# Optimization experiments

Hardware: AMD Instinct MI355X
Metric: run time of the kernel (lower is better)

Reference implementation:

```python
import jax, jax.numpy as jnp
import numpy as np
import math

N = 131072   # number of points
C = 32       # embed_dim
K = 19       # num_class
ZD = 16      # z_dim
BN_EPS = 1e-4
SIG_THR = 0.8


def setup_inputs():
    key = jax.random.key(0)
    ks = jax.random.split(key, 16)
    f32 = jnp.float32
    rn = lambda k, s, sc=1.0: jax.random.normal(k, s, dtype=f32) * sc
    return {
        'feat': rn(ks[0], (N, C)),
        'scene_flow': rn(ks[1], (N, 3)),
        'coarse_pred': rn(ks[2], (N, K)),
        'z': rn(ks[3], (ZD,)),
        'select_w1': rn(ks[4], (C, C), 0.2),
        'bn_gamma': jnp.ones((C,), f32),
        'bn_beta': jnp.zeros((C,), f32),
        'bn_mean': jnp.zeros((C,), f32),
        'bn_var': jnp.ones((C,), f32),
        'select_w2': rn(ks[5], (C, 1), 0.2),
        'select_b2': jnp.zeros((1,), f32),
        'wq': rn(ks[6], (C, C), 0.2), 'bq': jnp.zeros((C,), f32),
        'wk': rn(ks[7], (C, C), 0.2), 'bk': jnp.zeros((C,), f32),
        'wv': rn(ks[8], (C, C), 0.2), 'bv': jnp.zeros((C,), f32),
        'wo': rn(ks[9], (C, C), 0.2), 'bo': jnp.zeros((C,), f32),
        'wt': rn(ks[10], (2 * C, C), 0.2), 'bt': jnp.zeros((C,), f32),
        'w_out': rn(ks[11], (C, K), 0.2), 'b_out': jnp.zeros((K,), f32),
        'w_gen': rn(ks[12], (ZD + K + 3, C), 0.2), 'b_gen': jnp.zeros((C,), f32),
    }


def _forward(feat, scene_flow, coarse_pred, z, select_w1, bn_gamma, bn_beta,
             bn_mean, bn_var, select_w2, select_b2, wq, bq, wk, bk, wv, bv,
             wo, bo, wt, bt, w_out, b_out, w_gen, b_gen):
    cp = jax.nn.softmax(coarse_pred, axis=-1)                      # (N, K)
    temp_mask = jnp.any(scene_flow != 0, axis=-1)                  # (N,)
    # select_mlp: Linear(no bias) -> BatchNorm(eval, eps=1e-4) -> ReLU -> Linear -> Sigmoid
    h = (feat @ select_w1 - bn_mean) / jnp.sqrt(bn_var + BN_EPS) * bn_gamma + bn_beta
    h = jnp.maximum(h, 0.0)
    score = jax.nn.sigmoid(h @ select_w2 + select_b2)[:, 0]        # (N,)
    valid = (score < SIG_THR) & temp_mask                          # (N,)
    # cvae stand-in: linear over concat(z, onehot(class), scene_flow) -> (N, K, C)
    wz, wc, ws = w_gen[:ZD], w_gen[ZD:ZD + K], w_gen[ZD + K:]
    gen = (z @ wz + b_gen)[None, None, :] + wc[None, :, :] + (scene_flow @ ws)[:, None, :]
    gen = gen * cp[:, :, None]                                     # scale by softmax prob
    # tiny cross-attention: 1 query per point over K=19 class prototypes
    q = feat @ wq + bq                                             # (N, C)
    k_ = jnp.einsum('nkc,cd->nkd', gen, wk) + bk                   # (N, K, C)
    v_ = jnp.einsum('nkc,cd->nkd', gen, wv) + bv                   # (N, K, C)
    attn = jax.nn.softmax(jnp.einsum('nd,nkd->nk', q, k_) / math.sqrt(C), axis=-1)
    aug = jnp.einsum('nk,nkd->nd', attn, v_) @ wo + bo             # (N, C)
    # scatter-back: invalid points get zeros (equivalent to torch boolean scatter)
    new_feat = jnp.where(valid[:, None], aug, 0.0)
    refine = jnp.concatenate([feat, new_feat], axis=-1) @ wt + bt  # (N, C)
    return refine @ w_out + b_out                                  # (N, K)


def reference(feat, scene_flow, coarse_pred, z, select_w1, bn_gamma, bn_beta,
              bn_mean, bn_var, select_w2, select_b2, wq, bq, wk, bk, wv, bv,
              wo, bo, wt, bt, w_out, b_out, w_gen, b_gen):
    return _forward(feat, scene_flow, coarse_pred, z, select_w1, bn_gamma,
                    bn_beta, bn_mean, bn_var, select_w2, select_b2, wq, bq,
                    wk, bk, wv, bv, wo, bo, wt, bt, w_out, b_out, w_gen, b_gen)
```

## Files before the change

kernel.cpp:

```cpp
#include <hip/hip_runtime.h>

#define NPTS 131072

typedef __attribute__((ext_vector_type(8))) short short8;
typedef __attribute__((ext_vector_type(4))) float f32x4;

constexpr int OFF_SW1 = 0;
constexpr int OFF_BNS = 1024;
constexpr int OFF_BNH = 1056;
constexpr int OFF_SW2 = 1088;
constexpr int OFF_B2  = 1120;
constexpr int OFF_QGB = 1121;
constexpr int OFF_QMB = 1140;
constexpr int OFF_BB  = 1143;
constexpr int OFF_CV  = 1162;
constexpr int OFF_MVB = 1181;
constexpr int EGVB    = 1240;
constexpr int FRAGH   = 1620;
constexpr int FRAGL   = 2900;
constexpr int XA2 = 4020, XG = 4628, XMK = 5236, XMV = 5332;
constexpr int XGK = 5428, XGV = 6036, XB = 6644;

#define CONST_AS __attribute__((address_space(4)))
__device__ __forceinline__ const CONST_AS float* to_const(const float* p) {
    return (const CONST_AS float*)p;
}
__device__ __forceinline__ unsigned b16r(float x) {
    unsigned u = __float_as_uint(x);
    return (u + 0x7fffu + ((u >> 16) & 1u)) >> 16;
}
__device__ __forceinline__ float fromb(unsigned h) {
    return __uint_as_float(h << 16);
}
__device__ __forceinline__ int fragidx(int e, int col) {
    int T = col >> 4, l = (col & 15) + ((e >> 3) << 4), jj = e & 7;
    return (T * 64 + l) * 8 + jj;
}

__global__ __launch_bounds__(256) void pre_a(
    const float* __restrict__ z,
    const float* __restrict__ sw1,
    const float* __restrict__ bn_gamma, const float* __restrict__ bn_beta,
    const float* __restrict__ bn_mean,  const float* __restrict__ bn_var,
    const float* __restrict__ sw2,      const float* __restrict__ sb2,
    const float* __restrict__ wk, const float* __restrict__ wv,
    const float* __restrict__ wt, const float* __restrict__ bt,
    const float* __restrict__ wout, const float* __restrict__ bout,
    const float* __restrict__ wgen, const float* __restrict__ bgen,
    float* __restrict__ W)
{
    int i = blockIdx.x * 256 + threadIdx.x;
    unsigned short* FH = (unsigned short*)(W + FRAGH);
    unsigned short* FL = (unsigned short*)(W + FRAGL);
    if (i < 1024) {
        W[OFF_SW1 + i] = sw1[(i & 31) * 32 + (i >> 5)];
    } else if (i < 1632) {
        int t = i - 1024, e = t / 19, j = t % 19;
        float a1 = 0.f, a2 = 0.f;
        for (int d = 0; d < 32; ++d) {
            float w_ = wout[d*19 + j];
            a1 += wt[e*32 + d] * w_;
            a2 += wt[(32 + e)*32 + d] * w_;
        }
        FH[fragidx(e, 51 + j)] = (unsigned short)b16r(a1);
        W[XA2 + t] = a2;
    } else if (i < 2240) {
        int t = i - 1632, k = t >> 5, e = t & 31;
        float g = bgen[e];
        for (int d = 0; d < 16; ++d) g += z[d] * wgen[d*32 + e];
        W[XG + t] = g + wgen[(16 + k)*32 + e];
    } else if (i < 2336) {
        int t = i - 2240, m = t >> 5, c = t & 31;
        float a = 0.f, b = 0.f;
        for (int e = 0; e < 32; ++e) {
            float wsr = wgen[(35 + m)*32 + e];
            a += wsr * wk[e*32 + c];
            b += wsr * wv[e*32 + c];
        }
        W[XMK + t] = a; W[XMV + t] = b;
    } else if (i < 2368) {
        int t = i - 2336;
        float scale = bn_gamma[t] / sqrtf(bn_var[t] + 1e-4f);
        W[OFF_BNS + t] = scale;
        W[OFF_BNH + t] = bn_beta[t] - bn_mean[t] * scale;
        W[OFF_SW2 + t] = sw2[t];
    } else if (i < 2387) {
        int t = i - 2368;
        float a = bout[t];
        for (int d = 0; d < 32; ++d) a += bt[d] * wout[d*19 + t];
        W[OFF_BB + t] = a;
    } else if (i == 2387) {
        W[OFF_B2] = sb2[0];
    } else if (i < 3412) {
        int idx = i - 2388;
        int T = idx >> 9, rem = idx & 511, l = rem >> 3, j = rem & 7;
        int e = ((l >> 4) << 3) + j, col = 16*T + (l & 15);
        FH[(T*64 + l)*8 + j] = (unsigned short)b16r(sw1[e*32 + col]);
    } else if (i < 4436) {
        int idx = i - 3412;
        int T = idx >> 9, rem = idx & 511, l = rem >> 3, j = rem & 7;
        int e = ((l >> 4) << 3) + j, col = 16*T + (l & 15);
        float v = sw1[e*32 + col];
        FL[(T*64 + l)*8 + j] = (unsigned short)b16r(v - fromb(b16r(v)));
    } else if (i < 4660) {
        int idx = i - 4436;
        int col = 73 + idx / 32, rem = idx & 31, q = rem >> 3, j2 = rem & 7;
        int l = (col & 15) + (q << 4);
        FH[(4*64 + l)*8 + j2] = 0;
    }
}

__global__ __launch_bounds__(256) void pre_b(
    const float* __restrict__ wq, const float* __restrict__ bq,
    const float* __restrict__ wk, const float* __restrict__ wv,
    const float* __restrict__ wo,
    float* __restrict__ W)
{
    int i = blockIdx.x * 256 + threadIdx.x;
    unsigned short* FH = (unsigned short*)(W + FRAGH);
    if (i < 608) {
        int k = i >> 5, c = i & 31;
        float a = 0.f, b = 0.f;
        for (int e = 0; e < 32; ++e) {
            float g = W[XG + k*32 + e];
            a += g * wk[e*32 + c];
            b += g * wv[e*32 + c];
        }
        W[XGK + i] = a; W[XGV + i] = b;
    } else if (i < 1216) {
        int t = i - 608, c = t / 19, j = t % 19;
        float a = 0.f;
        for (int d = 0; d < 32; ++d) a += wo[c*32 + d] * W[XA2 + d*19 + j];
        W[XB + t] = a;
    } else if (i < 1312) {
        int t = i - 1216, e = t / 3, m = t % 3;
        float a = 0.f;
        for (int c = 0; c < 32; ++c) a += wq[e*32 + c] * W[XMK + m*32 + c];
        FH[fragidx(e, 70 + m)] = (unsigned short)b16r(a);
    } else if (i < 1315) {
        int m = i - 1312;
        float a = 0.f;
        for (int c = 0; c < 32; ++c) a += bq[c] * W[XMK + m*32 + c];
        W[OFF_QMB + m] = a;
    }
}

__global__ __launch_bounds__(256) void pre_c(
    const float* __restrict__ wq, const float* __restrict__ bq,
    const float* __restrict__ bv, const float* __restrict__ bo,
    float* __restrict__ W)
{
    int i = blockIdx.x * 256 + threadIdx.x;
    unsigned short* FH = (unsigned short*)(W + FRAGH);
    if (i < 608) {
        int e = i / 19, k = i % 19;
        float a = 0.f;
        for (int c = 0; c < 32; ++c) a += wq[e*32 + c] * W[XGK + k*32 + c];
        FH[fragidx(e, 32 + k)] = (unsigned short)b16r(a);
    } else if (i < 627) {
        int k = i - 608;
        float a = 0.f;
        for (int c = 0; c < 32; ++c) a += bq[c] * W[XGK + k*32 + c];
        W[OFF_QGB + k] = a;
    } else if (i < 988) {
        int t = i - 627, k = t / 19, j = t % 19;
        float a = 0.f;
        for (int c = 0; c < 32; ++c) a += W[XGV + k*32 + c] * W[XB + c*19 + j];
        W[EGVB + k*20 + j] = a;
    } else if (i < 1007) {
        int k = i - 988;
        W[EGVB + k*20 + 19] = 0.f;
    } else if (i < 1064) {
        int t = i - 1007, m = t / 19, j = t % 19;
        float a = 0.f;
        for (int c = 0; c < 32; ++c) a += W[XMV + m*32 + c] * W[XB + c*19 + j];
        W[OFF_MVB + t] = a;
    } else if (i < 1083) {
        int j = i - 1064;
        float a = 0.f;
        for (int c = 0; c < 32; ++c) a += bv[c] * W[XB + c*19 + j];
        for (int d = 0; d < 32; ++d) a += bo[d] * W[XA2 + d*19 + j];
        W[OFF_CV + j] = a;
    }
}

__global__ __launch_bounds__(256, 2) void main_k(
    const float* __restrict__ feat,
    const float* __restrict__ sflow,
    const float* __restrict__ cpred,
    const float* __restrict__ Wg,
    float* __restrict__ out)
{
    const CONST_AS float* W = to_const(Wg);
    const int t = threadIdx.x, lane = t & 63, wvi = t >> 6;
    const int pblk = blockIdx.x * 256;

    __shared__ __align__(16) float R0[32 * 264];
    __shared__ __align__(16) unsigned short OH[41 * 264];
    __shared__ __align__(16) float GV[380];

    if (t < 95) ((float4*)GV)[t] = ((const float4*)(Wg + EGVB))[t];

    {
        const float4* src = (const float4*)(cpred + (long)pblk * 19);
        float4* dst = (float4*)R0;
        dst[t] = src[t];
        dst[256 + t] = src[256 + t];
        dst[512 + t] = src[512 + t];
        dst[768 + t] = src[768 + t];
        if (t < 192) dst[1024 + t] = src[1024 + t];
    }
    __syncthreads();
    float cp[19];
#pragma unroll
    for (int k = 0; k < 19; ++k) cp[k] = R0[t*19 + k];
    float m1 = cp[0];
#pragma unroll
    for (int k = 1; k < 19; ++k) m1 = fmaxf(m1, cp[k]);
    float sum1 = 0.f;
#pragma unroll
    for (int k = 0; k < 19; ++k) { cp[k] = __expf(cp[k] - m1); sum1 += cp[k]; }
    float r1 = 1.f / sum1;
#pragma unroll
    for (int k = 0; k < 19; ++k) cp[k] *= r1;
    __syncthreads();

    const short8* FH8 = (const short8*)(Wg + FRAGH);
    const short8* FL8 = (const short8*)(Wg + FRAGL);
    short8 bh0 = FH8[0*64 + lane], bh1 = FH8[1*64 + lane];
    short8 bh2 = FH8[2*64 + lane], bh3 = FH8[3*64 + lane];
    short8 bh4 = FH8[4*64 + lane];
    short8 bl0 = FL8[0*64 + lane], bl1 = FL8[1*64 + lane];

    const int n15 = lane & 15, q = lane >> 4;

#pragma unroll
    for (int tile = 0; tile < 4; ++tile) {
        const int p0 = wvi*64 + tile*16;
        const float* fr = feat + (long)(pblk + p0 + n15) * 32 + q*8;
        float xv[8];
        {
            float4 va = *(const float4*)fr;
            float4 vb = *(const float4*)(fr + 4);
            xv[0]=va.x; xv[1]=va.y; xv[2]=va.z; xv[3]=va.w;
            xv[4]=vb.x; xv[5]=vb.y; xv[6]=vb.z; xv[7]=vb.w;
        }
        short8 ah, al;
#pragma unroll
        for (int j = 0; j < 8; ++j) {
            unsigned h = b16r(xv[j]);
            ah[j] = (short)h;
            al[j] = (short)b16r(xv[j] - fromb(h));
        }
        f32x4 z4 = {0.f, 0.f, 0.f, 0.f};
        f32x4 aH0, aH1, a2_, a3_, a4_;
        aH0 = __builtin_amdgcn_mfma_f32_16x16x32_bf16(ah, bh0, z4, 0, 0, 0);
        aH0 = __builtin_amdgcn_mfma_f32_16x16x32_bf16(ah, bl0, aH0, 0, 0, 0);
        aH0 = __builtin_amdgcn_mfma_f32_16x16x32_bf16(al, bh0, aH0, 0, 0, 0);
        aH1 = __builtin_amdgcn_mfma_f32_16x16x32_bf16(ah, bh1, z4, 0, 0, 0);
        aH1 = __builtin_amdgcn_mfma_f32_16x16x32_bf16(ah, bl1, aH1, 0, 0, 0);
        aH1 = __builtin_amdgcn_mfma_f32_16x16x32_bf16(al, bh1, aH1, 0, 0, 0);
        a2_ = __builtin_amdgcn_mfma_f32_16x16x32_bf16(ah, bh2, z4, 0, 0, 0);
        a3_ = __builtin_amdgcn_mfma_f32_16x16x32_bf16(ah, bh3, z4, 0, 0, 0);
        a4_ = __builtin_amdgcn_mfma_f32_16x16x32_bf16(ah, bh4, z4, 0, 0, 0);

        *(f32x4*)&R0[(n15)      * 264 + p0 + q*4] = aH0;
        *(f32x4*)&R0[(16 + n15) * 264 + p0 + q*4] = aH1;
        {
            unsigned d0, d1;
            d0 = b16r(a2_[0]) | (b16r(a2_[1]) << 16);
            d1 = b16r(a2_[2]) | (b16r(a2_[3]) << 16);
            *(uint2*)&OH[(n15) * 264 + p0 + q*4] = make_uint2(d0, d1);
            d0 = b16r(a3_[0]) | (b16r(a3_[1]) << 16);
            d1 = b16r(a3_[2]) | (b16r(a3_[3]) << 16);
            *(uint2*)&OH[(16 + n15) * 264 + p0 + q*4] = make_uint2(d0, d1);
            if (n15 <= 8) {
                d0 = b16r(a4_[0]) | (b16r(a4_[1]) << 16);
                d1 = b16r(a4_[2]) | (b16r(a4_[3]) << 16);
                *(uint2*)&OH[(32 + n15) * 264 + p0 + q*4] = make_uint2(d0, d1);
            }
        }
    }
    __syncthreads();

    const long p = pblk + t;

    float s0 = sflow[p*3 + 0], s1 = sflow[p*3 + 1], s2 = sflow[p*3 + 2];
    bool tmask = (s0 != 0.f) | (s1 != 0.f) | (s2 != 0.f);

    const float TH = 1.3862943611198906f;
    float sacc = W[OFF_B2];
#pragma unroll
    for (int c = 0; c < 32; ++c) {
        float a = R0[c*264 + t];
        float h = fmaxf(fmaf(a, W[OFF_BNS + c], W[OFF_BNH + c]), 0.f);
        sacc = fmaf(h, W[OFF_SW2 + c], sacc);
    }
    bool nearthr = fabsf(sacc - TH) < 1e-3f;
    if (__ballot(nearthr) != 0ULL) {
        float f[32];
        const float4* fp4 = (const float4*)(feat + p*32);
#pragma unroll
        for (int g = 0; g < 8; ++g) {
            float4 v = fp4[g];
            f[g*4+0]=v.x; f[g*4+1]=v.y; f[g*4+2]=v.z; f[g*4+3]=v.w;
        }
        float sr = W[OFF_B2];
        for (int c = 0; c < 32; ++c) {
            float a = 0.f;
#pragma unroll
            for (int e = 0; e < 32; ++e) a = fmaf(f[e], W[OFF_SW1 + c*32 + e], a);
            float h = fmaxf(fmaf(a, W[OFF_BNS + c], W[OFF_BNH + c]), 0.f);
            sr = fmaf(h, W[OFF_SW2 + c], sr);
        }
        sacc = nearthr ? sr : sacc;
    }
    bool valid = tmask && (sacc < TH);

    float qm0 = fromb(OH[38*264 + t]) + W[OFF_QMB + 0];
    float qm1 = fromb(OH[39*264 + t]) + W[OFF_QMB + 1];
    float qm2 = fromb(OH[40*264 + t]) + W[OFF_QMB + 2];
    float qs = s0*qm0 + s1*qm1 + s2*qm2;

    const float RS = 0.17677669529663687f;
    float l[19];
#pragma unroll
    for (int k = 0; k < 19; ++k)
        l[k] = (cp[k] * (fromb(OH[k*264 + t]) + W[OFF_QGB + k] + qs)) * RS;

    float m2 = l[0];
#pragma unroll
    for (int k = 1; k < 19; ++k) m2 = fmaxf(m2, l[k]);
    float sum2 = 0.f;
#pragma unroll
    for (int k = 0; k < 19; ++k) { l[k] = __expf(l[k] - m2); sum2 += l[k]; }
    float r2 = 1.f / sum2;
    float Sw = 0.f;
#pragma unroll
    for (int k = 0; k < 19; ++k) { l[k] = l[k] * r2 * cp[k]; Sw += l[k]; }

    float rv[19];
    float c0 = Sw * s0, c1 = Sw * s1, c2 = Sw * s2;
    float vg = valid ? 1.f : 0.f;
    float a2v[19];
#pragma unroll
    for (int j = 0; j < 19; ++j)
        a2v[j] = W[OFF_CV + j] + c0 * W[OFF_MVB + j]
               + c1 * W[OFF_MVB + 19 + j] + c2 * W[OFF_MVB + 38 + j];
#pragma unroll
    for (int k = 0; k < 19; ++k) {
        float lk = l[k];
#pragma unroll
        for (int j = 0; j < 19; ++j) a2v[j] = fmaf(lk, GV[k*20 + j], a2v[j]);
    }
#pragma unroll
    for (int j = 0; j < 19; ++j)
        rv[j] = fmaf(vg, a2v[j], fromb(OH[(19 + j)*264 + t]) + W[OFF_BB + j]);

    __syncthreads();
#pragma unroll
    for (int j = 0; j < 19; ++j) R0[t*19 + j] = rv[j];
    __syncthreads();
    {
        const float4* src = (const float4*)R0;
        float4* dst = (float4*)(out + (long)pblk * 19);
        dst[t] = src[t];
        dst[256 + t] = src[256 + t];
        dst[512 + t] = src[512 + t];
        dst[768 + t] = src[768 + t];
        if (t < 192) dst[1024 + t] = src[1024 + t];
    }
}

extern "C" void kernel_launch(void* const* d_in, const int* in_sizes, int n_in,
                              void* d_out, int out_size, void* d_ws, size_t ws_size,
                              hipStream_t stream) {
    const float* feat  = (const float*)d_in[0];
    const float* sflow = (const float*)d_in[1];
    const float* cpred = (const float*)d_in[2];
    const float* z     = (const float*)d_in[3];
    const float* sw1   = (const float*)d_in[4];
    const float* bn_g  = (const float*)d_in[5];
    const float* bn_b  = (const float*)d_in[6];
    const float* bn_m  = (const float*)d_in[7];
    const float* bn_v  = (const float*)d_in[8];
    const float* sw2   = (const float*)d_in[9];
    const float* sb2   = (const float*)d_in[10];
    const float* wq    = (const float*)d_in[11];
    const float* bq    = (const float*)d_in[12];
    const float* wk    = (const float*)d_in[13];
    const float* bk    = (const float*)d_in[14];  (void)bk;
    const float* wv    = (const float*)d_in[15];
    const float* bv    = (const float*)d_in[16];
    const float* wo    = (const float*)d_in[17];
    const float* bo    = (const float*)d_in[18];
    const float* wt    = (const float*)d_in[19];
    const float* bt    = (const float*)d_in[20];
    const float* wout  = (const float*)d_in[21];
    const float* bout  = (const float*)d_in[22];
    const float* wgen  = (const float*)d_in[23];
    const float* bgen  = (const float*)d_in[24];

    float* W = (float*)d_ws;

    hipLaunchKernelGGL(pre_a, dim3(19), dim3(256), 0, stream,
                       z, sw1, bn_g, bn_b, bn_m, bn_v, sw2, sb2,
                       wk, wv, wt, bt, wout, bout, wgen, bgen, W);
    hipLaunchKernelGGL(pre_b, dim3(6), dim3(256), 0, stream,
                       wq, bq, wk, wv, wo, W);
    hipLaunchKernelGGL(pre_c, dim3(5), dim3(256), 0, stream,
                       wq, bq, bv, bo, W);

    hipLaunchKernelGGL(main_k, dim3(512), dim3(256), 0, stream,
                       feat, sflow, cpred, W, (float*)d_out);
}
```

Measured before the change: 140.3 us.

## Merge weight-prep kernels into one block and fuse select score via shuffles

The three preprocessing kernels become a single 1024-thread block that keeps its intermediates in shared memory and separates phases with __syncthreads, removing two launches and the global round-trips between them. In the main kernel, the select-MLP score is reduced inside the MFMA tile loop with cross-lane shuffles instead of staging a 32x264 float buffer in LDS. The feature and scene-flow loads are issued early, and the output staging reuses the OH buffer, which shrinks LDS enough to raise occupancy to 3 blocks per CU. In exchange, preprocessing runs serially on one block, and register pressure rises from the prefetched features.

```diff
diff --git a/kernel.cpp b/kernel.cpp
--- a/kernel.cpp
+++ b/kernel.cpp
@@ -18,8 +18,6 @@
 constexpr int EGVB    = 1240;
 constexpr int FRAGH   = 1620;
 constexpr int FRAGL   = 2900;
-constexpr int XA2 = 4020, XG = 4628, XMK = 5236, XMV = 5332;
-constexpr int XGK = 5428, XGV = 6036, XB = 6644;
 
 #define CONST_AS __attribute__((address_space(4)))
 __device__ __forceinline__ const CONST_AS float* to_const(const float* p) {
@@ -37,154 +35,149 @@
     return (T * 64 + l) * 8 + jj;
 }
 
-__global__ __launch_bounds__(256) void pre_a(
+__global__ __launch_bounds__(1024) void pre_all(
     const float* __restrict__ z,
     const float* __restrict__ sw1,
     const float* __restrict__ bn_gamma, const float* __restrict__ bn_beta,
     const float* __restrict__ bn_mean,  const float* __restrict__ bn_var,
     const float* __restrict__ sw2,      const float* __restrict__ sb2,
+    const float* __restrict__ wq, const float* __restrict__ bq,
     const float* __restrict__ wk, const float* __restrict__ wv,
+    const float* __restrict__ bv,
+    const float* __restrict__ wo, const float* __restrict__ bo,
     const float* __restrict__ wt, const float* __restrict__ bt,
     const float* __restrict__ wout, const float* __restrict__ bout,
     const float* __restrict__ wgen, const float* __restrict__ bgen,
     float* __restrict__ W)
 {
-    int i = blockIdx.x * 256 + threadIdx.x;
+    __shared__ float XA2s[608], XGs[608], XMKs[96], XMVs[96];
+    __shared__ float XGKs[608], XGVs[608], XBs[608];
+    const int tid = threadIdx.x;
     unsigned short* FH = (unsigned short*)(W + FRAGH);
     unsigned short* FL = (unsigned short*)(W + FRAGL);
-    if (i < 1024) {
-        W[OFF_SW1 + i] = sw1[(i & 31) * 32 + (i >> 5)];
-    } else if (i < 1632) {
-        int t = i - 1024, e = t / 19, j = t % 19;
-        float a1 = 0.f, a2 = 0.f;
-        for (int d = 0; d < 32; ++d) {
-            float w_ = wout[d*19 + j];
-            a1 += wt[e*32 + d] * w_;
-            a2 += wt[(32 + e)*32 + d] * w_;
-        }
-        FH[fragidx(e, 51 + j)] = (unsigned short)b16r(a1);
-        W[XA2 + t] = a2;
-    } else if (i < 2240) {
-        int t = i - 1632, k = t >> 5, e = t & 31;
-        float g = bgen[e];
-        for (int d = 0; d < 16; ++d) g += z[d] * wgen[d*32 + e];
-        W[XG + t] = g + wgen[(16 + k)*32 + e];
-    } else if (i < 2336) {
-        int t = i - 2240, m = t >> 5, c = t & 31;
-        float a = 0.f, b = 0.f;
-        for (int e = 0; e < 32; ++e) {
-            float wsr = wgen[(35 + m)*32 + e];
-            a += wsr * wk[e*32 + c];
-            b += wsr * wv[e*32 + c];
-        }
-        W[XMK + t] = a; W[XMV + t] = b;
-    } else if (i < 2368) {
-        int t = i - 2336;
-        float scale = bn_gamma[t] / sqrtf(bn_var[t] + 1e-4f);
-        W[OFF_BNS + t] = scale;
-        W[OFF_BNH + t] = bn_beta[t] - bn_mean[t] * scale;
-        W[OFF_SW2 + t] = sw2[t];
-    } else if (i < 2387) {
-        int t = i - 2368;
-        float a = bout[t];
-        for (int d = 0; d < 32; ++d) a += bt[d] * wout[d*19 + t];
-        W[OFF_BB + t] = a;
-    } else if (i == 2387) {
-        W[OFF_B2] = sb2[0];
-    } else if (i < 3412) {
-        int idx = i - 2388;
-        int T = idx >> 9, rem = idx & 511, l = rem >> 3, j = rem & 7;
-        int e = ((l >> 4) << 3) + j, col = 16*T + (l & 15);
-        FH[(T*64 + l)*8 + j] = (unsigned short)b16r(sw1[e*32 + col]);
-    } else if (i < 4436) {
-        int idx = i - 3412;
-        int T = idx >> 9, rem = idx & 511, l = rem >> 3, j = rem & 7;
-        int e = ((l >> 4) << 3) + j, col = 16*T + (l & 15);
-        float v = sw1[e*32 + col];
-        FL[(T*64 + l)*8 + j] = (unsigned short)b16r(v - fromb(b16r(v)));
-    } else if (i < 4660) {
-        int idx = i - 4436;
-        int col = 73 + idx / 32, rem = idx & 31, q = rem >> 3, j2 = rem & 7;
-        int l = (col & 15) + (q << 4);
-        FH[(4*64 + l)*8 + j2] = 0;
-    }
-}
-
-__global__ __launch_bounds__(256) void pre_b(
-    const float* __restrict__ wq, const float* __restrict__ bq,
-    const float* __restrict__ wk, const float* __restrict__ wv,
-    const float* __restrict__ wo,
-    float* __restrict__ W)
-{
-    int i = blockIdx.x * 256 + threadIdx.x;
-    unsigned short* FH = (unsigned short*)(W + FRAGH);
-    if (i < 608) {
-        int k = i >> 5, c = i & 31;
-        float a = 0.f, b = 0.f;
-        for (int e = 0; e < 32; ++e) {
-            float g = W[XG + k*32 + e];
-            a += g * wk[e*32 + c];
-            b += g * wv[e*32 + c];
-        }
-        W[XGK + i] = a; W[XGV + i] = b;
-    } else if (i < 1216) {
-        int t = i - 608, c = t / 19, j = t % 19;
-        float a = 0.f;
-        for (int d = 0; d < 32; ++d) a += wo[c*32 + d] * W[XA2 + d*19 + j];
-        W[XB + t] = a;
-    } else if (i < 1312) {
-        int t = i - 1216, e = t / 3, m = t % 3;
-        float a = 0.f;
-        for (int c = 0; c < 32; ++c) a += wq[e*32 + c] * W[XMK + m*32 + c];
-        FH[fragidx(e, 70 + m)] = (unsigned short)b16r(a);
-    } else if (i < 1315) {
-        int m = i - 1312;
-        float a = 0.f;
-        for (int c = 0; c < 32; ++c) a += bq[c] * W[XMK + m*32 + c];
-        W[OFF_QMB + m] = a;
-    }
-}
-
-__global__ __launch_bounds__(256) void pre_c(
-    const float* __restrict__ wq, const float* __restrict__ bq,
-    const float* __restrict__ bv, const float* __restrict__ bo,
-    float* __restrict__ W)
-{
-    int i = blockIdx.x * 256 + threadIdx.x;
-    unsigned short* FH = (unsigned short*)(W + FRAGH);
-    if (i < 608) {
-        int e = i / 19, k = i % 19;
-        float a = 0.f;
-        for (int c = 0; c < 32; ++c) a += wq[e*32 + c] * W[XGK + k*32 + c];
-        FH[fragidx(e, 32 + k)] = (unsigned short)b16r(a);
-    } else if (i < 627) {
-        int k = i - 608;
-        float a = 0.f;
-        for (int c = 0; c < 32; ++c) a += bq[c] * W[XGK + k*32 + c];
-        W[OFF_QGB + k] = a;
-    } else if (i < 988) {
-        int t = i - 627, k = t / 19, j = t % 19;
-        float a = 0.f;
-        for (int c = 0; c < 32; ++c) a += W[XGV + k*32 + c] * W[XB + c*19 + j];
-        W[EGVB + k*20 + j] = a;
-    } else if (i < 1007) {
-        int k = i - 988;
-        W[EGVB + k*20 + 19] = 0.f;
-    } else if (i < 1064) {
-        int t = i - 1007, m = t / 19, j = t % 19;
-        float a = 0.f;
-        for (int c = 0; c < 32; ++c) a += W[XMV + m*32 + c] * W[XB + c*19 + j];
-        W[OFF_MVB + t] = a;
-    } else if (i < 1083) {
-        int j = i - 1064;
-        float a = 0.f;
-        for (int c = 0; c < 32; ++c) a += bv[c] * W[XB + c*19 + j];
-        for (int d = 0; d < 32; ++d) a += bo[d] * W[XA2 + d*19 + j];
-        W[OFF_CV + j] = a;
-    }
-}
-
-__global__ __launch_bounds__(256, 2) void main_k(
+
+    for (int i = tid; i < 4660; i += 1024) {
+        if (i < 1024) {
+            W[OFF_SW1 + i] = sw1[(i & 31) * 32 + (i >> 5)];
+        } else if (i < 1632) {
+            int t = i - 1024, e = t / 19, j = t % 19;
+            float a1 = 0.f, a2 = 0.f;
+            for (int d = 0; d < 32; ++d) {
+                float w_ = wout[d*19 + j];
+                a1 += wt[e*32 + d] * w_;
+                a2 += wt[(32 + e)*32 + d] * w_;
+            }
+            FH[fragidx(e, 51 + j)] = (unsigned short)b16r(a1);
+            XA2s[t] = a2;
+        } else if (i < 2240) {
+            int t = i - 1632, k = t >> 5, e = t & 31;
+            float g = bgen[e];
+            for (int d = 0; d < 16; ++d) g += z[d] * wgen[d*32 + e];
+            XGs[t] = g + wgen[(16 + k)*32 + e];
+        } else if (i < 2336) {
+            int t = i - 2240, m = t >> 5, c = t & 31;
+            float a = 0.f, b = 0.f;
+            for (int e = 0; e < 32; ++e) {
+                float wsr = wgen[(35 + m)*32 + e];
+                a += wsr * wk[e*32 + c];
+                b += wsr * wv[e*32 + c];
+            }
+            XMKs[t] = a; XMVs[t] = b;
+        } else if (i < 2368) {
+            int t = i - 2336;
+            float scale = bn_gamma[t] / sqrtf(bn_var[t] + 1e-4f);
+            W[OFF_BNS + t] = scale;
+            W[OFF_BNH + t] = bn_beta[t] - bn_mean[t] * scale;
+            W[OFF_SW2 + t] = sw2[t];
+        } else if (i < 2387) {
+            int t = i - 2368;
+            float a = bout[t];
+            for (int d = 0; d < 32; ++d) a += bt[d] * wout[d*19 + t];
+            W[OFF_BB + t] = a;
+        } else if (i == 2387) {
+            W[OFF_B2] = sb2[0];
+        } else if (i < 3412) {
+            int idx = i - 2388;
+            int T = idx >> 9, rem = idx & 511, l = rem >> 3, j = rem & 7;
+            int e = ((l >> 4) << 3) + j, col = 16*T + (l & 15);
+            FH[(T*64 + l)*8 + j] = (unsigned short)b16r(sw1[e*32 + col]);
+        } else if (i < 4436) {
+            int idx = i - 3412;
+            int T = idx >> 9, rem = idx & 511, l = rem >> 3, j = rem & 7;
+            int e = ((l >> 4) << 3) + j, col = 16*T + (l & 15);
+            float v = sw1[e*32 + col];
+            FL[(T*64 + l)*8 + j] = (unsigned short)b16r(v - fromb(b16r(v)));
+        } else {
+            int idx = i - 4436;
+            int col = 73 + idx / 32, rem = idx & 31, qq = rem >> 3, j2 = rem & 7;
+            int l = (col & 15) + (qq << 4);
+            FH[(4*64 + l)*8 + j2] = 0;
+        }
+    }
+    __syncthreads();
+    for (int i = tid; i < 1315; i += 1024) {
+        if (i < 608) {
+            int k = i >> 5, c = i & 31;
+            float a = 0.f, b = 0.f;
+            for (int e = 0; e < 32; ++e) {
+                float g = XGs[k*32 + e];
+                a += g * wk[e*32 + c];
+                b += g * wv[e*32 + c];
+            }
+            XGKs[i] = a; XGVs[i] = b;
+        } else if (i < 1216) {
+            int t2 = i - 608, c = t2 / 19, j = t2 % 19;
+            float a = 0.f;
+            for (int d = 0; d < 32; ++d) a += wo[c*32 + d] * XA2s[d*19 + j];
+            XBs[t2] = a;
+        } else if (i < 1312) {
+            int t2 = i - 1216, e = t2 / 3, m = t2 % 3;
+            float a = 0.f;
+            for (int c = 0; c < 32; ++c) a += wq[e*32 + c] * XMKs[m*32 + c];
+            FH[fragidx(e, 70 + m)] = (unsigned short)b16r(a);
+        } else {
+            int m = i - 1312;
+            float a = 0.f;
+            for (int c = 0; c < 32; ++c) a += bq[c] * XMKs[m*32 + c];
+            W[OFF_QMB + m] = a;
+        }
+    }
+    __syncthreads();
+    for (int i = tid; i < 1083; i += 1024) {
+        if (i < 608) {
+            int e = i / 19, k = i % 19;
+            float a = 0.f;
+            for (int c = 0; c < 32; ++c) a += wq[e*32 + c] * XGKs[k*32 + c];
+            FH[fragidx(e, 32 + k)] = (unsigned short)b16r(a);
+        } else if (i < 627) {
+            int k = i - 608;
+            float a = 0.f;
+            for (int c = 0; c < 32; ++c) a += bq[c] * XGKs[k*32 + c];
+            W[OFF_QGB + k] = a;
+        } else if (i < 988) {
+            int t2 = i - 627, k = t2 / 19, j = t2 % 19;
+            float a = 0.f;
+            for (int c = 0; c < 32; ++c) a += XGVs[k*32 + c] * XBs[c*19 + j];
+            W[EGVB + k*20 + j] = a;
+        } else if (i < 1007) {
+            int k = i - 988;
+            W[EGVB + k*20 + 19] = 0.f;
+        } else if (i < 1064) {
+            int t2 = i - 1007, m = t2 / 19, j = t2 % 19;
+            float a = 0.f;
+            for (int c = 0; c < 32; ++c) a += XMVs[m*32 + c] * XBs[c*19 + j];
+            W[OFF_MVB + t2] = a;
+        } else {
+            int j = i - 1064;
+            float a = 0.f;
+            for (int c = 0; c < 32; ++c) a += bv[c] * XBs[c*19 + j];
+            for (int d = 0; d < 32; ++d) a += bo[d] * XA2s[d*19 + j];
+            W[OFF_CV + j] = a;
+        }
+    }
+}
+
+__global__ __launch_bounds__(256, 3) void main_k(
     const float* __restrict__ feat,
     const float* __restrict__ sflow,
     const float* __restrict__ cpred,
@@ -194,37 +187,20 @@
     const CONST_AS float* W = to_const(Wg);
     const int t = threadIdx.x, lane = t & 63, wvi = t >> 6;
     const int pblk = blockIdx.x * 256;
-
-    __shared__ __align__(16) float R0[32 * 264];
+    const int n15 = lane & 15, q = lane >> 4;
+
     __shared__ __align__(16) unsigned short OH[41 * 264];
+    __shared__ __align__(16) float CP[256 * 19];
     __shared__ __align__(16) float GV[380];
-
-    if (t < 95) ((float4*)GV)[t] = ((const float4*)(Wg + EGVB))[t];
-
-    {
-        const float4* src = (const float4*)(cpred + (long)pblk * 19);
-        float4* dst = (float4*)R0;
-        dst[t] = src[t];
-        dst[256 + t] = src[256 + t];
-        dst[512 + t] = src[512 + t];
-        dst[768 + t] = src[768 + t];
-        if (t < 192) dst[1024 + t] = src[1024 + t];
-    }
-    __syncthreads();
-    float cp[19];
-#pragma unroll
-    for (int k = 0; k < 19; ++k) cp[k] = R0[t*19 + k];
-    float m1 = cp[0];
-#pragma unroll
-    for (int k = 1; k < 19; ++k) m1 = fmaxf(m1, cp[k]);
-    float sum1 = 0.f;
-#pragma unroll
-    for (int k = 0; k < 19; ++k) { cp[k] = __expf(cp[k] - m1); sum1 += cp[k]; }
-    float r1 = 1.f / sum1;
-#pragma unroll
-    for (int k = 0; k < 19; ++k) cp[k] *= r1;
-    __syncthreads();
-
+    __shared__ __align__(16) float SG[256];
+
+    float4 fva[4], fvb[4];
+#pragma unroll
+    for (int tile = 0; tile < 4; ++tile) {
+        const float* fr = feat + (long)(pblk + wvi*64 + tile*16 + n15) * 32 + q*8;
+        fva[tile] = *(const float4*)fr;
+        fvb[tile] = *(const float4*)(fr + 4);
+    }
     const short8* FH8 = (const short8*)(Wg + FRAGH);
     const short8* FL8 = (const short8*)(Wg + FRAGL);
     short8 bh0 = FH8[0*64 + lane], bh1 = FH8[1*64 + lane];
@@ -232,19 +208,45 @@
     short8 bh4 = FH8[4*64 + lane];
     short8 bl0 = FL8[0*64 + lane], bl1 = FL8[1*64 + lane];
 
-    const int n15 = lane & 15, q = lane >> 4;
+    const long p = pblk + t;
+    float s0 = sflow[p*3 + 0], s1 = sflow[p*3 + 1], s2 = sflow[p*3 + 2];
+
+    float bns0 = W[OFF_BNS + n15],      bnh0 = W[OFF_BNH + n15],      w20 = W[OFF_SW2 + n15];
+    float bns1 = W[OFF_BNS + 16 + n15], bnh1 = W[OFF_BNH + 16 + n15], w21 = W[OFF_SW2 + 16 + n15];
+
+    if (t < 95) ((float4*)GV)[t] = ((const float4*)(Wg + EGVB))[t];
+
+    {
+        const float4* src = (const float4*)(cpred + (long)pblk * 19);
+        float4* dst = (float4*)CP;
+        dst[t] = src[t];
+        dst[256 + t] = src[256 + t];
+        dst[512 + t] = src[512 + t];
+        dst[768 + t] = src[768 + t];
+        if (t < 192) dst[1024 + t] = src[1024 + t];
+    }
+    __syncthreads();
+    {
+        float cp[19];
+#pragma unroll
+        for (int k = 0; k < 19; ++k) cp[k] = CP[t*19 + k];
+        float m1 = cp[0];
+#pragma unroll
+        for (int k = 1; k < 19; ++k) m1 = fmaxf(m1, cp[k]);
+        float sum1 = 0.f;
+#pragma unroll
+        for (int k = 0; k < 19; ++k) { cp[k] = __expf(cp[k] - m1); sum1 += cp[k]; }
+        float r1 = 1.f / sum1;
+#pragma unroll
+        for (int k = 0; k < 19; ++k) CP[t*19 + k] = cp[k] * r1;
+    }
 
 #pragma unroll
     for (int tile = 0; tile < 4; ++tile) {
         const int p0 = wvi*64 + tile*16;
-        const float* fr = feat + (long)(pblk + p0 + n15) * 32 + q*8;
         float xv[8];
-        {
-            float4 va = *(const float4*)fr;
-            float4 vb = *(const float4*)(fr + 4);
-            xv[0]=va.x; xv[1]=va.y; xv[2]=va.z; xv[3]=va.w;
-            xv[4]=vb.x; xv[5]=vb.y; xv[6]=vb.z; xv[7]=vb.w;
-        }
+        xv[0]=fva[tile].x; xv[1]=fva[tile].y; xv[2]=fva[tile].z; xv[3]=fva[tile].w;
+        xv[4]=fvb[tile].x; xv[5]=fvb[tile].y; xv[6]=fvb[tile].z; xv[7]=fvb[tile].w;
         short8 ah, al;
 #pragma unroll
         for (int j = 0; j < 8; ++j) {
@@ -264,8 +266,32 @@
         a3_ = __builtin_amdgcn_mfma_f32_16x16x32_bf16(ah, bh3, z4, 0, 0, 0);
         a4_ = __builtin_amdgcn_mfma_f32_16x16x32_bf16(ah, bh4, z4, 0, 0, 0);
 
-        *(f32x4*)&R0[(n15)      * 264 + p0 + q*4] = aH0;
-        *(f32x4*)&R0[(16 + n15) * 264 + p0 + q*4] = aH1;
+        float g0, g1, g2, g3;
+        {
+            float h0, h1;
+            h0 = fmaxf(fmaf(aH0[0], bns0, bnh0), 0.f);
+            h1 = fmaxf(fmaf(aH1[0], bns1, bnh1), 0.f);
+            g0 = fmaf(h0, w20, h1 * w21);
+            h0 = fmaxf(fmaf(aH0[1], bns0, bnh0), 0.f);
+            h1 = fmaxf(fmaf(aH1[1], bns1, bnh1), 0.f);
+            g1 = fmaf(h0, w20, h1 * w21);
+            h0 = fmaxf(fmaf(aH0[2], bns0, bnh0), 0.f);
+            h1 = fmaxf(fmaf(aH1[2], bns1, bnh1), 0.f);
+            g2 = fmaf(h0, w20, h1 * w21);
+            h0 = fmaxf(fmaf(aH0[3], bns0, bnh0), 0.f);
+            h1 = fmaxf(fmaf(aH1[3], bns1, bnh1), 0.f);
+            g3 = fmaf(h0, w20, h1 * w21);
+        }
+#pragma unroll
+        for (int m = 1; m < 16; m <<= 1) {
+            g0 += __shfl_xor(g0, m, 64);
+            g1 += __shfl_xor(g1, m, 64);
+            g2 += __shfl_xor(g2, m, 64);
+            g3 += __shfl_xor(g3, m, 64);
+        }
+        if (n15 == 0)
+            *(float4*)&SG[p0 + q*4] = make_float4(g0, g1, g2, g3);
+
         {
             unsigned d0, d1;
             d0 = b16r(a2_[0]) | (b16r(a2_[1]) << 16);
@@ -283,19 +309,10 @@
     }
     __syncthreads();
 
-    const long p = pblk + t;
-
-    float s0 = sflow[p*3 + 0], s1 = sflow[p*3 + 1], s2 = sflow[p*3 + 2];
     bool tmask = (s0 != 0.f) | (s1 != 0.f) | (s2 != 0.f);
 
     const float TH = 1.3862943611198906f;
-    float sacc = W[OFF_B2];
-#pragma unroll
-    for (int c = 0; c < 32; ++c) {
-        float a = R0[c*264 + t];
-        float h = fmaxf(fmaf(a, W[OFF_BNS + c], W[OFF_BNH + c]), 0.f);
-        sacc = fmaf(h, W[OFF_SW2 + c], sacc);
-    }
+    float sacc = SG[t] + W[OFF_B2];
     bool nearthr = fabsf(sacc - TH) < 1e-3f;
     if (__ballot(nearthr) != 0ULL) {
         float f[32];
@@ -322,6 +339,10 @@
     float qm2 = fromb(OH[40*264 + t]) + W[OFF_QMB + 2];
     float qs = s0*qm0 + s1*qm1 + s2*qm2;
 
+    float cp[19];
+#pragma unroll
+    for (int k = 0; k < 19; ++k) cp[k] = CP[t*19 + k];
+
     const float RS = 0.17677669529663687f;
     float l[19];
 #pragma unroll
@@ -358,11 +379,12 @@
         rv[j] = fmaf(vg, a2v[j], fromb(OH[(19 + j)*264 + t]) + W[OFF_BB + j]);
 
     __syncthreads();
-#pragma unroll
-    for (int j = 0; j < 19; ++j) R0[t*19 + j] = rv[j];
+    float* SLAB = (float*)OH;
+#pragma unroll
+    for (int j = 0; j < 19; ++j) SLAB[t*19 + j] = rv[j];
     __syncthreads();
     {
-        const float4* src = (const float4*)R0;
+        const float4* src = (const float4*)SLAB;
         float4* dst = (float4*)(out + (long)pblk * 19);
         dst[t] = src[t];
         dst[256 + t] = src[256 + t];
@@ -403,13 +425,10 @@
 
     float* W = (float*)d_ws;
 
-    hipLaunchKernelGGL(pre_a, dim3(19), dim3(256), 0, stream,
+    hipLaunchKernelGGL(pre_all, dim3(1), dim3(1024), 0, stream,
                        z, sw1, bn_g, bn_b, bn_m, bn_v, sw2, sb2,
-                       wk, wv, wt, bt, wout, bout, wgen, bgen, W);
-    hipLaunchKernelGGL(pre_b, dim3(6), dim3(256), 0, stream,
-                       wq, bq, wk, wv, wo, W);
-    hipLaunchKernelGGL(pre_c, dim3(5), dim3(256), 0, stream,
-                       wq, bq, bv, bo, W);
+                       wq, bq, wk, wv, bv, wo, bo, wt, bt, wout, bout,
+                       wgen, bgen, W);
 
     hipLaunchKernelGGL(main_k, dim3(512), dim3(256), 0, stream,
                        feat, sflow, cpred, W, (float*)d_out);
```

New measurement: 146.2 us. +4.2%, slower.
